# Kernel optimization log

Measured on AMD Instinct MI355X. Metric: run time of the kernel, lower is better.

## Reference

```python
import jax, jax.numpy as jnp
import numpy as np

OUT = 7   # output_size
SR = 2    # sampling_ratio
SCALES = (0.25, 0.125, 0.0625, 0.03125)  # inferred from feat sizes vs 800x800 image
K_MIN, LVL0, S0, EPS = 2, 4.0, 224.0, 1e-6


def _bilinear_gather(feat, b, y, x):
    """Legacy (aligned=False) bilinear sampling. feat [B,C,H,W]; b,y,x same shape S.
    Returns [*S, C]."""
    B, C, H, W = feat.shape
    valid = (y >= -1.0) & (y <= H) & (x >= -1.0) & (x <= W)
    y = jnp.maximum(y, 0.0)
    x = jnp.maximum(x, 0.0)
    yl = y.astype(jnp.int32)
    xl = x.astype(jnp.int32)
    ycond = yl >= H - 1
    yl = jnp.where(ycond, H - 1, yl)
    yh = jnp.where(ycond, H - 1, yl + 1)
    y = jnp.where(ycond, yl.astype(y.dtype), y)
    xcond = xl >= W - 1
    xl = jnp.where(xcond, W - 1, xl)
    xh = jnp.where(xcond, W - 1, xl + 1)
    x = jnp.where(xcond, xl.astype(x.dtype), x)
    ly = y - yl
    lx = x - xl
    hy = 1.0 - ly
    hx = 1.0 - lx
    def g(yy, xx):
        return feat[b, :, yy, xx]  # advanced indexing -> [*S, C]
    val = ((hy * hx)[..., None] * g(yl, xl)
           + (hy * lx)[..., None] * g(yl, xh)
           + (ly * hx)[..., None] * g(yh, xl)
           + (ly * lx)[..., None] * g(yh, xh))
    return jnp.where(valid[..., None], val, 0.0)


def _roi_align(feat, bidx, boxes, scale):
    """RoIAlign (aligned=False). feat [B,C,H,W], bidx [R] int, boxes [R,4] image coords.
    Returns [R,C,OUT,OUT]."""
    x1 = boxes[:, 0] * scale
    y1 = boxes[:, 1] * scale
    x2 = boxes[:, 2] * scale
    y2 = boxes[:, 3] * scale
    roi_w = jnp.maximum(x2 - x1, 1.0)
    roi_h = jnp.maximum(y2 - y1, 1.0)
    bin_h = roi_h / OUT
    bin_w = roi_w / OUT
    off = (jnp.arange(SR, dtype=feat.dtype) + 0.5) / SR      # [SR]
    ph = jnp.arange(OUT, dtype=feat.dtype)                   # [OUT]
    grid = ph[None, :, None] + off[None, None, :]            # [1,OUT,SR]
    ys = y1[:, None, None] + grid * bin_h[:, None, None]     # [R,OUT,SR]
    xs = x1[:, None, None] + grid * bin_w[:, None, None]     # [R,OUT,SR]
    Y = ys[:, :, None, :, None]                              # [R,OUT,1,SR,1]
    X = xs[:, None, :, None, :]                              # [R,1,OUT,1,SR]
    Yb, Xb = jnp.broadcast_arrays(Y, X)                      # [R,OUT,OUT,SR,SR]
    b = jnp.broadcast_to(bidx[:, None, None, None, None], Yb.shape)
    val = _bilinear_gather(feat, b, Yb, Xb)                  # [R,OUT,OUT,SR,SR,C]
    pooled = val.mean(axis=(3, 4))                           # [R,OUT,OUT,C]
    return jnp.transpose(pooled, (0, 3, 1, 2))               # [R,C,OUT,OUT]


def _levels(boxes_flat):
    """LevelMapper.run: FPN level index (0-based) per RoI."""
    area = (boxes_flat[:, 2] - boxes_flat[:, 0]) * (boxes_flat[:, 3] - boxes_flat[:, 1])
    s = jnp.sqrt(area)
    lvl = jnp.floor(LVL0 + jnp.log2(s / S0 + EPS))
    return jnp.clip(lvl, K_MIN, K_MIN + 3).astype(jnp.int32) - K_MIN


def setup_inputs() -> dict:
    key = jax.random.key(0)
    ks = jax.random.split(key, 6)
    sizes = [200, 100, 50, 25]
    inp = {f"feat{i}": jax.random.normal(ks[i], (2, 256, s, s), dtype=jnp.float32)
           for i, s in enumerate(sizes)}
    xy = jax.random.uniform(ks[4], (2, 256, 2), dtype=jnp.float32) * 500.0
    wh = jax.random.uniform(ks[5], (2, 256, 2), dtype=jnp.float32) * 400.0 + 8.0
    inp["boxes"] = jnp.concatenate([xy, xy + wh], axis=-1)  # (x1,y1,x2,y2) in [0,908)
    return inp


def reference(feat0, feat1, feat2, feat3, boxes):
    feats = [feat0, feat1, feat2, feat3]
    B, N, _ = boxes.shape
    bf = boxes.reshape(B * N, 4)
    bidx = jnp.repeat(jnp.arange(B, dtype=jnp.int32), N)  # convert_to_roi_format ids
    lv = _levels(bf)
    C = feats[0].shape[1]
    out = jnp.zeros((B * N, C, OUT, OUT), dtype=feats[0].dtype)
    for level, (f, sc) in enumerate(zip(feats, SCALES)):
        r = _roi_align(f, bidx, bf, sc)
        out = jnp.where((lv == level)[:, None, None, None], r, out)
    return out
```

## Files before the change

kernel.cpp:

```cpp
#include <hip/hip_runtime.h>

#define OUT 7
#define NCH 256
#define NROI 512
#define NS 14
#define CCH 16
#define PLANE 901
#define TPR (NCH * OUT * OUT)

__device__ __forceinline__ float rfl_f(float v) {
    return __int_as_float(__builtin_amdgcn_readfirstlane(__float_as_int(v)));
}

__device__ __forceinline__ unsigned int cvt_pk_bf16(float lo, float hi) {
    unsigned int r;
    asm("v_cvt_pk_bf16_f32 %0, %1, %2" : "=v"(r) : "v"(lo), "v"(hi));
    return r;
}

__device__ __forceinline__ void tap1d(float start, float bin, int sidx, int H,
                                      int& lo, int& hi, float& fr, float& vv) {
    int p = sidx >> 1, half = sidx & 1;
    float c = start + ((float)p + (half ? 0.75f : 0.25f)) * bin;
    vv = (c >= -1.0f && c <= (float)H) ? 0.5f : 0.0f;
    c = fmaxf(c, 0.0f);
    int l = (int)c;
    if (l >= H - 1) { lo = H - 1; hi = H - 1; fr = 0.0f; }
    else            { lo = l;     hi = l + 1; fr = c - (float)l; }
}

__global__ __launch_bounds__(256, 4) void roi_align_fp_kernel(
        const float* __restrict__ f0, const float* __restrict__ f1,
        const float* __restrict__ f2, const float* __restrict__ f3,
        const float* __restrict__ boxes, float* __restrict__ out) {
    __shared__ __align__(16) unsigned int sm32[8 * PLANE];
    __shared__ float lyS[NS], vyS[NS], lxS[NS], vxS[NS];
    __shared__ int rowLrel[NS], rowHrel[NS], colLrel[NS], colHrel[NS];

    int g    = blockIdx.x;
    int xcd  = g & 7;
    int slot = g >> 3;
    int rr_  = slot >> 4;
    int q    = slot & 15;
    int r    = rr_ * 8 + xcd;
    int tid  = (int)threadIdx.x;

    float bx1 = rfl_f(boxes[r * 4 + 0]);
    float by1 = rfl_f(boxes[r * 4 + 1]);
    float bx2 = rfl_f(boxes[r * 4 + 2]);
    float by2 = rfl_f(boxes[r * 4 + 3]);

    float area = (bx2 - bx1) * (by2 - by1);
    float s    = sqrtf(area);
    float lvl  = floorf(4.0f + log2f(s * (1.0f / 224.0f) + 1e-6f));
    lvl        = fminf(fmaxf(lvl, 2.0f), 5.0f);
    int level  = __builtin_amdgcn_readfirstlane((int)lvl - 2);

    const float* f; int H; float scale;
    switch (level) {
        case 0:  f = f0; H = 200; scale = 0.25f;    break;
        case 1:  f = f1; H = 100; scale = 0.125f;   break;
        case 2:  f = f2; H = 50;  scale = 0.0625f;  break;
        default: f = f3; H = 25;  scale = 0.03125f; break;
    }

    float x1 = bx1 * scale, y1 = by1 * scale;
    float roi_w = fmaxf(bx2 * scale - x1, 1.0f);
    float roi_h = fmaxf(by2 * scale - y1, 1.0f);
    float bin_w = roi_w * (1.0f / OUT);
    float bin_h = roi_h * (1.0f / OUT);

    int lo0, hi0, lo13, hi13; float frT, vvT;
    tap1d(y1, bin_h, 0,  H, lo0, hi0, frT, vvT);
    tap1d(y1, bin_h, 13, H, lo13, hi13, frT, vvT);
    int rowMin = __builtin_amdgcn_readfirstlane(lo0);
    int rowMax = __builtin_amdgcn_readfirstlane(hi13);
    tap1d(x1, bin_w, 0,  H, lo0, hi0, frT, vvT);
    tap1d(x1, bin_w, 13, H, lo13, hi13, frT, vvT);
    int colMin = __builtin_amdgcn_readfirstlane(lo0);
    int colMax = __builtin_amdgcn_readfirstlane(hi13);
    int Ht = rowMax - rowMin + 1;
    int Wd = colMax - colMin + 1;

    if (tid < NS) {
        int lo, hi; float fr, vv;
        tap1d(y1, bin_h, tid, H, lo, hi, fr, vv);
        lyS[tid] = fr; vyS[tid] = vv;
        rowLrel[tid] = lo - rowMin; rowHrel[tid] = hi - rowMin;
    } else if (tid >= 32 && tid < 32 + NS) {
        int t = tid - 32;
        int lo, hi; float fr, vv;
        tap1d(x1, bin_w, t, H, lo, hi, fr, vv);
        lxS[t] = fr; vxS[t] = vv;
        colLrel[t] = lo - colMin; colHrel[t] = hi - colMin;
    }

    int bidx = r >> 8;
    size_t HH = (size_t)(H * H);
    int lane = tid & 63;
    int wv   = __builtin_amdgcn_readfirstlane(tid >> 6);

    const float* pw0 = f + ((size_t)(bidx * NCH + q * CCH + 4 * wv)) * HH
                         + (size_t)(rowMin * H + colMin);
    size_t HH1 = HH, HH2 = 2 * HH, HH3 = 3 * HH;
    int wb0 = (2 * wv) * PLANE;
    int wb1 = wb0 + PLANE;

    bool TWO = (Wd > 64);
    int  cA  = (lane < Wd) ? lane : (Wd - 1);
    int  cB  = TWO ? ((lane + 64 < Wd) ? lane + 64 : Wd - 1) : 0;
    bool wA  = (lane < Wd);
    bool wB  = TWO && (lane + 64 < Wd);

#define DECLS(s) float A##s, B##s, C##s, D##s, E##s = 0, F##s = 0, G##s = 0, I##s = 0;
    DECLS(0) DECLS(1) DECLS(2) DECLS(3)

#define STG_ISSUE(s, rv) { \
        int rr = (rv) < Ht ? (rv) : (Ht - 1); \
        const float* p = pw0 + (size_t)(rr * H); \
        A##s = p[cA]; B##s = p[HH1 + cA]; C##s = p[HH2 + cA]; D##s = p[HH3 + cA]; \
        if (TWO) { E##s = p[cB]; F##s = p[HH1 + cB]; G##s = p[HH2 + cB]; I##s = p[HH3 + cB]; } }

#define STG_CONSUME(s, rv) { \
        if ((rv) < Ht) { \
            int wb = (rv) * Wd + lane; \
            if (wA) { \
                sm32[wb0 + wb] = cvt_pk_bf16(A##s, B##s); \
                sm32[wb1 + wb] = cvt_pk_bf16(C##s, D##s); } \
            if (wB) { \
                sm32[wb0 + wb + 64] = cvt_pk_bf16(E##s, F##s); \
                sm32[wb1 + wb + 64] = cvt_pk_bf16(G##s, I##s); } } }

    STG_ISSUE(0, 0) STG_ISSUE(1, 1) STG_ISSUE(2, 2) STG_ISSUE(3, 3)
    for (int rw = 0; rw < Ht; rw += 4) {
        STG_CONSUME(0, rw)     STG_ISSUE(0, rw + 4)
        STG_CONSUME(1, rw + 1) STG_ISSUE(1, rw + 5)
        STG_CONSUME(2, rw + 2) STG_ISSUE(2, rw + 6)
        STG_CONSUME(3, rw + 3) STG_ISSUE(3, rw + 7)
    }
    __syncthreads();

    float accx[2], accy[2];
#pragma unroll
    for (int i = 0; i < 2; ++i) { accx[i] = 0.0f; accy[i] = 0.0f; }

#pragma unroll
    for (int i = 0; i < 2; ++i) {
        int o = tid + 256 * i;
        if (o < 392) {
            int cp = o & 7, px = o >> 3;
            int ph = px / 7, pw = px - ph * 7;
            int cpP = cp * PLANE;
            float ax = 0.0f, ay = 0.0f;
#pragma unroll
            for (int iy = 0; iy < 2; ++iy) {
                int sy = ph * 2 + iy;
                float ly = lyS[sy], hy = 1.0f - ly;
                float vy = vyS[sy];
                int rL = cpP + rowLrel[sy] * Wd;
                int rH = cpP + rowHrel[sy] * Wd;
#pragma unroll
                for (int ix = 0; ix < 2; ++ix) {
                    int sx = pw * 2 + ix;
                    float lx = lxS[sx], hx = 1.0f - lx;
                    float m  = vy * vxS[sx];
                    int cL = colLrel[sx], cH = colHrel[sx];
                    unsigned int u00 = sm32[rL + cL];
                    unsigned int u01 = sm32[rL + cH];
                    unsigned int u10 = sm32[rH + cL];
                    unsigned int u11 = sm32[rH + cH];
                    float w00 = hy * hx * m, w01 = hy * lx * m;
                    float w10 = ly * hx * m, w11 = ly * lx * m;
                    ax = fmaf(w00, __uint_as_float(u00 << 16), ax);
                    ay = fmaf(w00, __uint_as_float(u00 & 0xFFFF0000u), ay);
                    ax = fmaf(w01, __uint_as_float(u01 << 16), ax);
                    ay = fmaf(w01, __uint_as_float(u01 & 0xFFFF0000u), ay);
                    ax = fmaf(w10, __uint_as_float(u10 << 16), ax);
                    ay = fmaf(w10, __uint_as_float(u10 & 0xFFFF0000u), ay);
                    ax = fmaf(w11, __uint_as_float(u11 << 16), ax);
                    ay = fmaf(w11, __uint_as_float(u11 & 0xFFFF0000u), ay);
                }
            }
            accx[i] = ax; accy[i] = ay;
        }
    }
    __syncthreads();

    float* smf = (float*)sm32;
#pragma unroll
    for (int i = 0; i < 2; ++i) {
        int o = tid + 256 * i;
        if (o < 392) {
            int cp = o & 7, px = o >> 3;
            smf[(cp * 2 + 0) * 49 + px] = accx[i];
            smf[(cp * 2 + 1) * 49 + px] = accy[i];
        }
    }
    __syncthreads();

    float* dst = out + (size_t)r * TPR + (size_t)q * (CCH * 49);
    if (tid < 196)
        ((float4*)dst)[tid] = ((const float4*)smf)[tid];
}

extern "C" void kernel_launch(void* const* d_in, const int* in_sizes, int n_in,
                              void* d_out, int out_size, void* d_ws, size_t ws_size,
                              hipStream_t stream) {
    const float* f0    = (const float*)d_in[0];
    const float* f1    = (const float*)d_in[1];
    const float* f2    = (const float*)d_in[2];
    const float* f3    = (const float*)d_in[3];
    const float* boxes = (const float*)d_in[4];
    float* out         = (float*)d_out;

    roi_align_fp_kernel<<<NROI * 16, 256, 0, stream>>>(f0, f1, f2, f3, boxes, out);
}
```

Before: 194.1 us.

## Halve channels per block and stage feature patch with flattened pixel loop

Each block now handles 8 channels instead of 16, doubling the grid to 16384 blocks and halving the shared-memory tile so more blocks can be resident per CU. The row-wise software-pipelined staging with two column passes is replaced by a flat loop over all patch pixels, where each lane computes row and column by integer division and loads two channel planes. Shared-memory plane size grows so larger patches fit. The compute phase drops to one output element per thread with only 196 of 256 threads active. The cost is more block overhead, repeated box/tap setup per block, and losing the explicit multi-row load prefetch.

```diff
diff --git a/kernel.cpp b/kernel.cpp
--- a/kernel.cpp
+++ b/kernel.cpp
@@ -4,8 +4,8 @@
 #define NCH 256
 #define NROI 512
 #define NS 14
-#define CCH 16
-#define PLANE 901
+#define CCH 8
+#define PLANE 1151
 #define TPR (NCH * OUT * OUT)
 
 __device__ __forceinline__ float rfl_f(float v) {
@@ -29,19 +29,19 @@
     else            { lo = l;     hi = l + 1; fr = c - (float)l; }
 }
 
-__global__ __launch_bounds__(256, 4) void roi_align_fp_kernel(
+__global__ __launch_bounds__(256, 8) void roi_align_fpd_kernel(
         const float* __restrict__ f0, const float* __restrict__ f1,
         const float* __restrict__ f2, const float* __restrict__ f3,
         const float* __restrict__ boxes, float* __restrict__ out) {
-    __shared__ __align__(16) unsigned int sm32[8 * PLANE];
+    __shared__ __align__(16) unsigned int sm32[4 * PLANE];
     __shared__ float lyS[NS], vyS[NS], lxS[NS], vxS[NS];
     __shared__ int rowLrel[NS], rowHrel[NS], colLrel[NS], colHrel[NS];
 
     int g    = blockIdx.x;
     int xcd  = g & 7;
     int slot = g >> 3;
-    int rr_  = slot >> 4;
-    int q    = slot & 15;
+    int rr_  = slot >> 5;
+    int q    = slot & 31;
     int r    = rr_ * 8 + xcd;
     int tid  = (int)threadIdx.x;
 
@@ -81,6 +81,7 @@
     int colMax = __builtin_amdgcn_readfirstlane(hi13);
     int Ht = rowMax - rowMin + 1;
     int Wd = colMax - colMin + 1;
+    int P  = Ht * Wd;
 
     if (tid < NS) {
         int lo, hi; float fr, vv;
@@ -100,106 +101,74 @@
     int lane = tid & 63;
     int wv   = __builtin_amdgcn_readfirstlane(tid >> 6);
 
-    const float* pw0 = f + ((size_t)(bidx * NCH + q * CCH + 4 * wv)) * HH
-                         + (size_t)(rowMin * H + colMin);
-    size_t HH1 = HH, HH2 = 2 * HH, HH3 = 3 * HH;
-    int wb0 = (2 * wv) * PLANE;
-    int wb1 = wb0 + PLANE;
+    const float* pa = f + ((size_t)(bidx * NCH + q * CCH + 2 * wv)) * HH
+                        + (size_t)(rowMin * H + colMin);
+    const float* pb = pa + HH;
+    int wb = wv * PLANE;
+    unsigned uWd = (unsigned)Wd;
 
-    bool TWO = (Wd > 64);
-    int  cA  = (lane < Wd) ? lane : (Wd - 1);
-    int  cB  = TWO ? ((lane + 64 < Wd) ? lane + 64 : Wd - 1) : 0;
-    bool wA  = (lane < Wd);
-    bool wB  = TWO && (lane + 64 < Wd);
-
-#define DECLS(s) float A##s, B##s, C##s, D##s, E##s = 0, F##s = 0, G##s = 0, I##s = 0;
-    DECLS(0) DECLS(1) DECLS(2) DECLS(3)
-
-#define STG_ISSUE(s, rv) { \
-        int rr = (rv) < Ht ? (rv) : (Ht - 1); \
-        const float* p = pw0 + (size_t)(rr * H); \
-        A##s = p[cA]; B##s = p[HH1 + cA]; C##s = p[HH2 + cA]; D##s = p[HH3 + cA]; \
-        if (TWO) { E##s = p[cB]; F##s = p[HH1 + cB]; G##s = p[HH2 + cB]; I##s = p[HH3 + cB]; } }
-
-#define STG_CONSUME(s, rv) { \
-        if ((rv) < Ht) { \
-            int wb = (rv) * Wd + lane; \
-            if (wA) { \
-                sm32[wb0 + wb] = cvt_pk_bf16(A##s, B##s); \
-                sm32[wb1 + wb] = cvt_pk_bf16(C##s, D##s); } \
-            if (wB) { \
-                sm32[wb0 + wb + 64] = cvt_pk_bf16(E##s, F##s); \
-                sm32[wb1 + wb + 64] = cvt_pk_bf16(G##s, I##s); } } }
-
-    STG_ISSUE(0, 0) STG_ISSUE(1, 1) STG_ISSUE(2, 2) STG_ISSUE(3, 3)
-    for (int rw = 0; rw < Ht; rw += 4) {
-        STG_CONSUME(0, rw)     STG_ISSUE(0, rw + 4)
-        STG_CONSUME(1, rw + 1) STG_ISSUE(1, rw + 5)
-        STG_CONSUME(2, rw + 2) STG_ISSUE(2, rw + 6)
-        STG_CONSUME(3, rw + 3) STG_ISSUE(3, rw + 7)
+    for (int p0 = 0; p0 < P; p0 += 64) {
+        int p  = p0 + lane;
+        int pc = (p < P) ? p : (P - 1);
+        unsigned rw = (unsigned)pc / uWd;
+        unsigned cl = (unsigned)pc - rw * uWd;
+        size_t off  = (size_t)rw * (size_t)H + (size_t)cl;
+        float a = pa[off];
+        float b = pb[off];
+        if (p < P) sm32[wb + p] = cvt_pk_bf16(a, b);
     }
     __syncthreads();
 
-    float accx[2], accy[2];
+    float accx = 0.0f, accy = 0.0f;
+    int o = tid;
+    if (o < 196) {
+        int cp = o & 3, px = o >> 2;
+        int ph = px / 7, pw2 = px - ph * 7;
+        int cpP = cp * PLANE;
+        float ax = 0.0f, ay = 0.0f;
 #pragma unroll
-    for (int i = 0; i < 2; ++i) { accx[i] = 0.0f; accy[i] = 0.0f; }
-
+        for (int iy = 0; iy < 2; ++iy) {
+            int sy = ph * 2 + iy;
+            float ly = lyS[sy], hy = 1.0f - ly;
+            float vy = vyS[sy];
+            int rL = cpP + rowLrel[sy] * Wd;
+            int rH = cpP + rowHrel[sy] * Wd;
 #pragma unroll
-    for (int i = 0; i < 2; ++i) {
-        int o = tid + 256 * i;
-        if (o < 392) {
-            int cp = o & 7, px = o >> 3;
-            int ph = px / 7, pw = px - ph * 7;
-            int cpP = cp * PLANE;
-            float ax = 0.0f, ay = 0.0f;
-#pragma unroll
-            for (int iy = 0; iy < 2; ++iy) {
-                int sy = ph * 2 + iy;
-                float ly = lyS[sy], hy = 1.0f - ly;
-                float vy = vyS[sy];
-                int rL = cpP + rowLrel[sy] * Wd;
-                int rH = cpP + rowHrel[sy] * Wd;
-#pragma unroll
-                for (int ix = 0; ix < 2; ++ix) {
-                    int sx = pw * 2 + ix;
-                    float lx = lxS[sx], hx = 1.0f - lx;
-                    float m  = vy * vxS[sx];
-                    int cL = colLrel[sx], cH = colHrel[sx];
-                    unsigned int u00 = sm32[rL + cL];
-                    unsigned int u01 = sm32[rL + cH];
-                    unsigned int u10 = sm32[rH + cL];
-                    unsigned int u11 = sm32[rH + cH];
-                    float w00 = hy * hx * m, w01 = hy * lx * m;
-                    float w10 = ly * hx * m, w11 = ly * lx * m;
-                    ax = fmaf(w00, __uint_as_float(u00 << 16), ax);
-                    ay = fmaf(w00, __uint_as_float(u00 & 0xFFFF0000u), ay);
-                    ax = fmaf(w01, __uint_as_float(u01 << 16), ax);
-                    ay = fmaf(w01, __uint_as_float(u01 & 0xFFFF0000u), ay);
-                    ax = fmaf(w10, __uint_as_float(u10 << 16), ax);
-                    ay = fmaf(w10, __uint_as_float(u10 & 0xFFFF0000u), ay);
-                    ax = fmaf(w11, __uint_as_float(u11 << 16), ax);
-                    ay = fmaf(w11, __uint_as_float(u11 & 0xFFFF0000u), ay);
-                }
+            for (int ix = 0; ix < 2; ++ix) {
+                int sx = pw2 * 2 + ix;
+                float lx = lxS[sx], hx = 1.0f - lx;
+                float m  = vy * vxS[sx];
+                int cL = colLrel[sx], cH = colHrel[sx];
+                unsigned int u00 = sm32[rL + cL];
+                unsigned int u01 = sm32[rL + cH];
+                unsigned int u10 = sm32[rH + cL];
+                unsigned int u11 = sm32[rH + cH];
+                float w00 = hy * hx * m, w01 = hy * lx * m;
+                float w10 = ly * hx * m, w11 = ly * lx * m;
+                ax = fmaf(w00, __uint_as_float(u00 << 16), ax);
+                ay = fmaf(w00, __uint_as_float(u00 & 0xFFFF0000u), ay);
+                ax = fmaf(w01, __uint_as_float(u01 << 16), ax);
+                ay = fmaf(w01, __uint_as_float(u01 & 0xFFFF0000u), ay);
+                ax = fmaf(w10, __uint_as_float(u10 << 16), ax);
+                ay = fmaf(w10, __uint_as_float(u10 & 0xFFFF0000u), ay);
+                ax = fmaf(w11, __uint_as_float(u11 << 16), ax);
+                ay = fmaf(w11, __uint_as_float(u11 & 0xFFFF0000u), ay);
             }
-            accx[i] = ax; accy[i] = ay;
         }
+        accx = ax; accy = ay;
     }
     __syncthreads();
 
     float* smf = (float*)sm32;
-#pragma unroll
-    for (int i = 0; i < 2; ++i) {
-        int o = tid + 256 * i;
-        if (o < 392) {
-            int cp = o & 7, px = o >> 3;
-            smf[(cp * 2 + 0) * 49 + px] = accx[i];
-            smf[(cp * 2 + 1) * 49 + px] = accy[i];
-        }
+    if (o < 196) {
+        int cp = o & 3, px = o >> 2;
+        smf[(cp * 2 + 0) * 49 + px] = accx;
+        smf[(cp * 2 + 1) * 49 + px] = accy;
     }
     __syncthreads();
 
     float* dst = out + (size_t)r * TPR + (size_t)q * (CCH * 49);
-    if (tid < 196)
+    if (tid < 98)
         ((float4*)dst)[tid] = ((const float4*)smf)[tid];
 }
 
@@ -213,5 +182,5 @@
     const float* boxes = (const float*)d_in[4];
     float* out         = (float*)d_out;
 
-    roi_align_fp_kernel<<<NROI * 16, 256, 0, stream>>>(f0, f1, f2, f3, boxes, out);
+    roi_align_fpd_kernel<<<NROI * 32, 256, 0, stream>>>(f0, f1, f2, f3, boxes, out);
 }
```

After: 194.6 us. Within noise of the previous version (+0.3%).
